# Optimization experiments

Hardware: AMD Instinct MI355X
Metric: run time of the kernel (lower is better)

Reference implementation:

```python
import jax, jax.numpy as jnp
import numpy as np

B, F_SIZE, DIM = 2048, 32, 64
LAYER_SIZES = (128, 128)


def setup_inputs() -> dict:
    key = jax.random.key(0)
    k1, k2, k3 = jax.random.split(key, 3)
    inputs = jax.random.normal(k1, (B, F_SIZE, DIM), dtype=jnp.float32)
    # Conv1d(kernel=1) weights: (out_channels, in_channels)
    W0 = jax.random.normal(k2, (128, F_SIZE * F_SIZE), dtype=jnp.float32) * 0.03
    b0 = jnp.zeros((128,), dtype=jnp.float32)
    # split_half -> field_nums[1] = 64 -> in_channels = 64 * 32 = 2048
    W1 = jax.random.normal(k3, (128, 64 * F_SIZE), dtype=jnp.float32) * 0.03
    b1 = jnp.zeros((128,), dtype=jnp.float32)
    return {"inputs": inputs, "W0": W0, "b0": b0, "W1": W1, "b1": b1}


def _cin_forward(inputs, Ws, bs):
    batch, _, dim = inputs.shape
    x0 = inputs
    h = inputs
    finals = []
    n_layers = len(Ws)
    for i in range(n_layers):
        H = h.shape[1]
        M = x0.shape[1]
        # outer-product interaction: (b, H, M, d) -> (b, H*M, d)
        z = jnp.einsum('bhd,bmd->bhmd', h, x0).reshape(batch, H * M, dim)
        # 1x1 conv == per-position channel matmul
        out = jnp.einsum('bcd,oc->bod', z, Ws[i]) + bs[i][None, :, None]
        out = jax.nn.relu(out)
        size = Ws[i].shape[0]
        if i != n_layers - 1:
            # split_half: first half feeds next layer, second half is output
            h = out[:, : size // 2, :]
            finals.append(out[:, size // 2 :, :])
        else:
            finals.append(out)
    result = jnp.concatenate(finals, axis=1)  # (b, 64 + 128, d)
    return jnp.sum(result, axis=-1)           # (b, 192)


def reference(inputs, W0, b0, W1, b1):
    return _cin_forward(inputs, (W0, W1), (b0, b1))
```

## Files before the change

kernel.cpp:

```cpp
#include <hip/hip_runtime.h>


#define BATCH 2048
#define FSZ   32
#define DIM   64
#define K0    1024
#define K1    2048
#define OUTC  192

#define W0_ELEMS (128 * K0)
#define W1_ELEMS (128 * K1)
#define TOT_ELEMS (W0_ELEMS + W1_ELEMS)
#define CVT_THREADS (TOT_ELEMS / 4)

typedef _Float16 v8h  __attribute__((ext_vector_type(8)));
typedef float    v16f __attribute__((ext_vector_type(16)));

#define XT_PITCH 40
#define XD_PITCH 66
#define HD_PITCH 66

__global__ void convert_w_kernel(const float* __restrict__ W0,
                                 const float* __restrict__ W1,
                                 _Float16* __restrict__ wsw) {
    int t = blockIdx.x * blockDim.x + threadIdx.x;
    if (t >= CVT_THREADS) return;
    int e = t * 4;
    const float* src;
    if (e < W0_ELEMS) {
        int f = e >> 3, j0 = e & 7;
        int ks = f >> 8, ob = (f >> 6) & 3, lane = f & 63;
        src = W0 + (size_t)(ob * 32 + (lane & 31)) * K0
                 + ks * 16 + (lane >> 5) * 8 + j0;
    } else {
        int u = e - W0_ELEMS;
        int f = u >> 3, j0 = u & 7;
        int ks = f >> 8, ob = (f >> 6) & 3, lane = f & 63;
        src = W1 + (size_t)(ob * 32 + (lane & 31)) * K1
                 + ks * 16 + (lane >> 5) * 8 + j0;
    }
    float4 v = *(const float4*)src;
    _Float16* dst = wsw + e;
    dst[0] = (_Float16)v.x;
    dst[1] = (_Float16)v.y;
    dst[2] = (_Float16)v.z;
    dst[3] = (_Float16)v.w;
}

__global__ __launch_bounds__(256, 4) void cin_kernel(
    const float* __restrict__ X,
    const float* __restrict__ b0,
    const float* __restrict__ b1,
    const _Float16* __restrict__ Wsw,
    float* __restrict__ out)
{
    __shared__ _Float16 xT[DIM * XT_PITCH];
    __shared__ _Float16 xD[FSZ * XD_PITCH];
    __shared__ _Float16 h1D[64 * HD_PITCH];

    const int b    = blockIdx.x;
    const int tid  = threadIdx.x;
    const int wave = tid >> 6;
    const int lane = tid & 63;
    const int half = lane >> 5;
    const int d0   = lane & 31;

    const float* xb = X + (size_t)b * (FSZ * DIM);
    #pragma unroll
    for (int i = tid; i < FSZ * DIM; i += 256) {
        int m = i >> 6, d = i & 63;
        _Float16 v = (_Float16)xb[i];
        xT[d * XT_PITCH + m] = v;
        xD[m * XD_PITCH + d] = v;
    }
    __syncthreads();

    v8h xh[2][2];
    #pragma unroll
    for (int db = 0; db < 2; ++db)
        #pragma unroll
        for (int p = 0; p < 2; ++p)
            xh[db][p] = *(const v8h*)(&xT[(db * 32 + d0) * XT_PITCH + p * 16 + half * 8]);

    v16f acc0 = (v16f)0.0f;
    v16f acc1 = (v16f)0.0f;

    {
        const _Float16* Wk = Wsw + (size_t)(wave * 64 + lane) * 8;
        #pragma unroll 4
        for (int ks = 0; ks < 64; ++ks) {
            v8h a = *(const v8h*)(Wk + (size_t)ks * 2048);
            const int hr = ks >> 1;
            _Float16 s0 = xD[hr * XD_PITCH + d0];
            _Float16 s1 = xD[hr * XD_PITCH + 32 + d0];
            v8h s08 = {s0, s0, s0, s0, s0, s0, s0, s0};
            v8h s18 = {s1, s1, s1, s1, s1, s1, s1, s1};
            v8h bf0 = s08 * xh[0][ks & 1];
            v8h bf1 = s18 * xh[1][ks & 1];
            acc0 = __builtin_amdgcn_mfma_f32_32x32x16_f16(a, bf0, acc0, 0, 0, 0);
            acc1 = __builtin_amdgcn_mfma_f32_32x32x16_f16(a, bf1, acc1, 0, 0, 0);
        }
    }

    if (wave < 2) {
        #pragma unroll
        for (int reg = 0; reg < 16; ++reg) {
            const int o = wave * 32 + (reg & 3) + 8 * (reg >> 2) + 4 * half;
            const float bias = b0[o];
            float v0 = acc0[reg] + bias; v0 = v0 > 0.0f ? v0 : 0.0f;
            float v1 = acc1[reg] + bias; v1 = v1 > 0.0f ? v1 : 0.0f;
            h1D[o * HD_PITCH + d0]      = (_Float16)v0;
            h1D[o * HD_PITCH + 32 + d0] = (_Float16)v1;
        }
    } else {
        #pragma unroll
        for (int reg = 0; reg < 16; ++reg) {
            const int o = wave * 32 + (reg & 3) + 8 * (reg >> 2) + 4 * half;
            const float bias = b0[o];
            float v0 = acc0[reg] + bias; v0 = v0 > 0.0f ? v0 : 0.0f;
            float v1 = acc1[reg] + bias; v1 = v1 > 0.0f ? v1 : 0.0f;
            float s = v0 + v1;
            s += __shfl_xor(s, 1);
            s += __shfl_xor(s, 2);
            s += __shfl_xor(s, 4);
            s += __shfl_xor(s, 8);
            s += __shfl_xor(s, 16);
            if (d0 == 0) out[(size_t)b * OUTC + (o - 64)] = s;
        }
    }
    __syncthreads();

    acc0 = (v16f)0.0f;
    acc1 = (v16f)0.0f;

    {
        const _Float16* Wk = Wsw + W0_ELEMS + (size_t)(wave * 64 + lane) * 8;
        #pragma unroll 4
        for (int ks = 0; ks < 128; ++ks) {
            v8h a = *(const v8h*)(Wk + (size_t)ks * 2048);
            const int hr = ks >> 1;
            _Float16 s0 = h1D[hr * HD_PITCH + d0];
            _Float16 s1 = h1D[hr * HD_PITCH + 32 + d0];
            v8h s08 = {s0, s0, s0, s0, s0, s0, s0, s0};
            v8h s18 = {s1, s1, s1, s1, s1, s1, s1, s1};
            v8h bf0 = s08 * xh[0][ks & 1];
            v8h bf1 = s18 * xh[1][ks & 1];
            acc0 = __builtin_amdgcn_mfma_f32_32x32x16_f16(a, bf0, acc0, 0, 0, 0);
            acc1 = __builtin_amdgcn_mfma_f32_32x32x16_f16(a, bf1, acc1, 0, 0, 0);
        }
    }

    #pragma unroll
    for (int reg = 0; reg < 16; ++reg) {
        const int o = wave * 32 + (reg & 3) + 8 * (reg >> 2) + 4 * half;
        const float bias = b1[o];
        float v0 = acc0[reg] + bias; v0 = v0 > 0.0f ? v0 : 0.0f;
        float v1 = acc1[reg] + bias; v1 = v1 > 0.0f ? v1 : 0.0f;
        float s = v0 + v1;
        s += __shfl_xor(s, 1);
        s += __shfl_xor(s, 2);
        s += __shfl_xor(s, 4);
        s += __shfl_xor(s, 8);
        s += __shfl_xor(s, 16);
        if (d0 == 0) out[(size_t)b * OUTC + 64 + o] = s;
    }
}

extern "C" void kernel_launch(void* const* d_in, const int* in_sizes, int n_in,
                              void* d_out, int out_size, void* d_ws, size_t ws_size,
                              hipStream_t stream) {
    const float* X  = (const float*)d_in[0];
    const float* W0 = (const float*)d_in[1];
    const float* b0 = (const float*)d_in[2];
    const float* W1 = (const float*)d_in[3];
    const float* b1 = (const float*)d_in[4];
    float* out = (float*)d_out;
    _Float16* wsw = (_Float16*)d_ws;

    convert_w_kernel<<<(CVT_THREADS + 255) / 256, 256, 0, stream>>>(W0, W1, wsw);
    cin_kernel<<<BATCH, 256, 0, stream>>>(X, b0, b1, wsw, out);
}
```

Measured before the change: 179.6 us.

## Process two batch items per block with 2x2 MFMA tiles and prefetched weights

Each block now handles two batch elements. Waves split by batch item and output-row half, and each wave computes a 2x2 grid of 32x32 MFMA tiles, so every weight fragment loaded from global memory is reused across two output slices. The weight layout is re-swizzled to match. Weight and scalar loads for the next k-step are software-prefetched into registers, and the LDS layouts for x and h1 are interleaved so each lane fetches both d-halves with a single packed load. The cost is twice as many accumulator registers and half as many blocks, which can lower occupancy and latency hiding.

```diff
diff --git a/kernel.cpp b/kernel.cpp
--- a/kernel.cpp
+++ b/kernel.cpp
@@ -13,12 +13,11 @@
 #define TOT_ELEMS (W0_ELEMS + W1_ELEMS)
 #define CVT_THREADS (TOT_ELEMS / 4)
 
-typedef _Float16 v8h  __attribute__((ext_vector_type(8)));
+typedef _Float16 v8h __attribute__((ext_vector_type(8)));
+typedef _Float16 v2h __attribute__((ext_vector_type(2)));
 typedef float    v16f __attribute__((ext_vector_type(16)));
 
 #define XT_PITCH 40
-#define XD_PITCH 66
-#define HD_PITCH 66
 
 __global__ void convert_w_kernel(const float* __restrict__ W0,
                                  const float* __restrict__ W1,
@@ -27,24 +26,28 @@
     if (t >= CVT_THREADS) return;
     int e = t * 4;
     const float* src;
+    _Float16* dst;
     if (e < W0_ELEMS) {
-        int f = e >> 3, j0 = e & 7;
-        int ks = f >> 8, ob = (f >> 6) & 3, lane = f & 63;
-        src = W0 + (size_t)(ob * 32 + (lane & 31)) * K0
+        int j0 = e & 7, lane = (e >> 3) & 63, s = (e >> 9) & 3, ks = e >> 11;
+        src = W0 + (size_t)(s * 32 + (lane & 31)) * K0
                  + ks * 16 + (lane >> 5) * 8 + j0;
+        dst = wsw + e;
     } else {
         int u = e - W0_ELEMS;
-        int f = u >> 3, j0 = u & 7;
-        int ks = f >> 8, ob = (f >> 6) & 3, lane = f & 63;
-        src = W1 + (size_t)(ob * 32 + (lane & 31)) * K1
+        int j0 = u & 7, lane = (u >> 3) & 63, s = (u >> 9) & 3, ks = u >> 11;
+        src = W1 + (size_t)(s * 32 + (lane & 31)) * K1
                  + ks * 16 + (lane >> 5) * 8 + j0;
+        dst = wsw + W0_ELEMS + u;
     }
     float4 v = *(const float4*)src;
-    _Float16* dst = wsw + e;
     dst[0] = (_Float16)v.x;
     dst[1] = (_Float16)v.y;
     dst[2] = (_Float16)v.z;
     dst[3] = (_Float16)v.w;
+}
+
+__device__ __forceinline__ v16f mfma32(v8h a, v8h b, v16f c) {
+    return __builtin_amdgcn_mfma_f32_32x32x16_f16(a, b, c, 0, 0, 0);
 }
 
 __global__ __launch_bounds__(256, 4) void cin_kernel(
@@ -54,115 +57,174 @@
     const _Float16* __restrict__ Wsw,
     float* __restrict__ out)
 {
-    __shared__ _Float16 xT[DIM * XT_PITCH];
-    __shared__ _Float16 xD[FSZ * XD_PITCH];
-    __shared__ _Float16 h1D[64 * HD_PITCH];
-
-    const int b    = blockIdx.x;
+    __shared__ _Float16 xT[2][DIM * XT_PITCH];
+    __shared__ _Float16 xP[2][FSZ * 64];
+    __shared__ _Float16 h1P[2][64 * 64];
+
+    const int b0i  = blockIdx.x * 2;
     const int tid  = threadIdx.x;
     const int wave = tid >> 6;
     const int lane = tid & 63;
-    const int half = lane >> 5;
+    const int p    = wave & 1;
+    const int rh   = wave >> 1;
     const int d0   = lane & 31;
-
-    const float* xb = X + (size_t)b * (FSZ * DIM);
+    const int hi   = lane >> 5;
+
     #pragma unroll
-    for (int i = tid; i < FSZ * DIM; i += 256) {
-        int m = i >> 6, d = i & 63;
-        _Float16 v = (_Float16)xb[i];
-        xT[d * XT_PITCH + m] = v;
-        xD[m * XD_PITCH + d] = v;
+    for (int i = 0; i < 4; ++i) {
+        int idx = tid + i * 256;
+        int pp = idx >> 9, r4 = idx & 511;
+        float4 v = *(const float4*)(X + (size_t)(b0i + pp) * (FSZ * DIM) + r4 * 4);
+        int m = (r4 * 4) >> 6, d = (r4 * 4) & 63;
+        int g = d >> 5, c = d & 31;
+        _Float16 f0 = (_Float16)v.x, f1 = (_Float16)v.y,
+                 f2 = (_Float16)v.z, f3 = (_Float16)v.w;
+        xT[pp][(d + 0) * XT_PITCH + m] = f0;
+        xT[pp][(d + 1) * XT_PITCH + m] = f1;
+        xT[pp][(d + 2) * XT_PITCH + m] = f2;
+        xT[pp][(d + 3) * XT_PITCH + m] = f3;
+        xP[pp][m * 64 + (c + 0) * 2 + g] = f0;
+        xP[pp][m * 64 + (c + 1) * 2 + g] = f1;
+        xP[pp][m * 64 + (c + 2) * 2 + g] = f2;
+        xP[pp][m * 64 + (c + 3) * 2 + g] = f3;
     }
     __syncthreads();
 
-    v8h xh[2][2];
+    v8h xw[2][2];
     #pragma unroll
-    for (int db = 0; db < 2; ++db)
-        #pragma unroll
-        for (int p = 0; p < 2; ++p)
-            xh[db][p] = *(const v8h*)(&xT[(db * 32 + d0) * XT_PITCH + p * 16 + half * 8]);
-
-    v16f acc0 = (v16f)0.0f;
-    v16f acc1 = (v16f)0.0f;
+    for (int g = 0; g < 2; ++g)
+        #pragma unroll
+        for (int q = 0; q < 2; ++q)
+            xw[g][q] = *(const v8h*)(&xT[p][(g * 32 + d0) * XT_PITCH + q * 16 + hi * 8]);
+
+    const _Float16* Wb0 = Wsw + (size_t)rh * 1024 + (size_t)lane * 8;
+    const _Float16* Wb1 = Wb0 + W0_ELEMS;
+    const _Float16* xPp = &xP[p][d0 * 2];
+    const _Float16* hPp = &h1P[p][d0 * 2];
+
+    v16f acc[2][2];
+    acc[0][0] = (v16f)0.0f; acc[0][1] = (v16f)0.0f;
+    acc[1][0] = (v16f)0.0f; acc[1][1] = (v16f)0.0f;
 
     {
-        const _Float16* Wk = Wsw + (size_t)(wave * 64 + lane) * 8;
-        #pragma unroll 4
-        for (int ks = 0; ks < 64; ++ks) {
-            v8h a = *(const v8h*)(Wk + (size_t)ks * 2048);
-            const int hr = ks >> 1;
-            _Float16 s0 = xD[hr * XD_PITCH + d0];
-            _Float16 s1 = xD[hr * XD_PITCH + 32 + d0];
+        v8h A0, A1, A2, A3, N0, N1, N2, N3;
+        v2h svC, svN;
+        A0 = *(const v8h*)(Wb0);        A1 = *(const v8h*)(Wb0 + 512);
+        A2 = *(const v8h*)(Wb0 + 2048); A3 = *(const v8h*)(Wb0 + 2560);
+        svC = *(const v2h*)(xPp);
+        #pragma unroll 1
+        for (int i = 0; i < 32; ++i) {
+            const int kn = (i + 1) & 31;
+            const _Float16* Wn = Wb0 + (size_t)kn * 4096;
+            N0 = *(const v8h*)(Wn);        N1 = *(const v8h*)(Wn + 512);
+            N2 = *(const v8h*)(Wn + 2048); N3 = *(const v8h*)(Wn + 2560);
+            svN = *(const v2h*)(xPp + kn * 64);
+            _Float16 s0 = svC[0], s1 = svC[1];
             v8h s08 = {s0, s0, s0, s0, s0, s0, s0, s0};
             v8h s18 = {s1, s1, s1, s1, s1, s1, s1, s1};
-            v8h bf0 = s08 * xh[0][ks & 1];
-            v8h bf1 = s18 * xh[1][ks & 1];
-            acc0 = __builtin_amdgcn_mfma_f32_32x32x16_f16(a, bf0, acc0, 0, 0, 0);
-            acc1 = __builtin_amdgcn_mfma_f32_32x32x16_f16(a, bf1, acc1, 0, 0, 0);
-        }
-    }
-
-    if (wave < 2) {
+            v8h be0 = s08 * xw[0][0];
+            v8h be1 = s18 * xw[1][0];
+            acc[0][0] = mfma32(A0, be0, acc[0][0]);
+            acc[1][0] = mfma32(A1, be0, acc[1][0]);
+            acc[0][1] = mfma32(A0, be1, acc[0][1]);
+            acc[1][1] = mfma32(A1, be1, acc[1][1]);
+            v8h bo0 = s08 * xw[0][1];
+            v8h bo1 = s18 * xw[1][1];
+            acc[0][0] = mfma32(A2, bo0, acc[0][0]);
+            acc[1][0] = mfma32(A3, bo0, acc[1][0]);
+            acc[0][1] = mfma32(A2, bo1, acc[0][1]);
+            acc[1][1] = mfma32(A3, bo1, acc[1][1]);
+            A0 = N0; A1 = N1; A2 = N2; A3 = N3;
+            svC = svN;
+        }
+    }
+
+    if (rh == 0) {
+        #pragma unroll
+        for (int sl = 0; sl < 2; ++sl) {
+            #pragma unroll
+            for (int reg = 0; reg < 16; ++reg) {
+                const int o = sl * 32 + (reg & 3) + 8 * (reg >> 2) + 4 * hi;
+                const float bias = b0[o];
+                float v0 = acc[sl][0][reg] + bias; v0 = v0 > 0.0f ? v0 : 0.0f;
+                float v1 = acc[sl][1][reg] + bias; v1 = v1 > 0.0f ? v1 : 0.0f;
+                v2h pk = {(_Float16)v0, (_Float16)v1};
+                *(v2h*)(&h1P[p][o * 64 + d0 * 2]) = pk;
+            }
+        }
+    } else {
+        #pragma unroll
+        for (int sl = 0; sl < 2; ++sl) {
+            #pragma unroll
+            for (int reg = 0; reg < 16; ++reg) {
+                const int o = 64 + sl * 32 + (reg & 3) + 8 * (reg >> 2) + 4 * hi;
+                const float bias = b0[o];
+                float v0 = acc[sl][0][reg] + bias; v0 = v0 > 0.0f ? v0 : 0.0f;
+                float v1 = acc[sl][1][reg] + bias; v1 = v1 > 0.0f ? v1 : 0.0f;
+                float s = v0 + v1;
+                s += __shfl_xor(s, 1);
+                s += __shfl_xor(s, 2);
+                s += __shfl_xor(s, 4);
+                s += __shfl_xor(s, 8);
+                s += __shfl_xor(s, 16);
+                if (d0 == 0) out[(size_t)(b0i + p) * OUTC + (o - 64)] = s;
+            }
+        }
+    }
+    __syncthreads();
+
+    acc[0][0] = (v16f)0.0f; acc[0][1] = (v16f)0.0f;
+    acc[1][0] = (v16f)0.0f; acc[1][1] = (v16f)0.0f;
+
+    {
+        v8h A0, A1, A2, A3, N0, N1, N2, N3;
+        v2h svC, svN;
+        A0 = *(const v8h*)(Wb1);        A1 = *(const v8h*)(Wb1 + 512);
+        A2 = *(const v8h*)(Wb1 + 2048); A3 = *(const v8h*)(Wb1 + 2560);
+        svC = *(const v2h*)(hPp);
+        #pragma unroll 1
+        for (int i = 0; i < 64; ++i) {
+            const int kn = (i + 1) & 63;
+            const _Float16* Wn = Wb1 + (size_t)kn * 4096;
+            N0 = *(const v8h*)(Wn);        N1 = *(const v8h*)(Wn + 512);
+            N2 = *(const v8h*)(Wn + 2048); N3 = *(const v8h*)(Wn + 2560);
+            svN = *(const v2h*)(hPp + kn * 64);
+            _Float16 s0 = svC[0], s1 = svC[1];
+            v8h s08 = {s0, s0, s0, s0, s0, s0, s0, s0};
+            v8h s18 = {s1, s1, s1, s1, s1, s1, s1, s1};
+            v8h be0 = s08 * xw[0][0];
+            v8h be1 = s18 * xw[1][0];
+            acc[0][0] = mfma32(A0, be0, acc[0][0]);
+            acc[1][0] = mfma32(A1, be0, acc[1][0]);
+            acc[0][1] = mfma32(A0, be1, acc[0][1]);
+            acc[1][1] = mfma32(A1, be1, acc[1][1]);
+            v8h bo0 = s08 * xw[0][1];
+            v8h bo1 = s18 * xw[1][1];
+            acc[0][0] = mfma32(A2, bo0, acc[0][0]);
+            acc[1][0] = mfma32(A3, bo0, acc[1][0]);
+            acc[0][1] = mfma32(A2, bo1, acc[0][1]);
+            acc[1][1] = mfma32(A3, bo1, acc[1][1]);
+            A0 = N0; A1 = N1; A2 = N2; A3 = N3;
+            svC = svN;
+        }
+    }
+
+    #pragma unroll
+    for (int sl = 0; sl < 2; ++sl) {
         #pragma unroll
         for (int reg = 0; reg < 16; ++reg) {
-            const int o = wave * 32 + (reg & 3) + 8 * (reg >> 2) + 4 * half;
-            const float bias = b0[o];
-            float v0 = acc0[reg] + bias; v0 = v0 > 0.0f ? v0 : 0.0f;
-            float v1 = acc1[reg] + bias; v1 = v1 > 0.0f ? v1 : 0.0f;
-            h1D[o * HD_PITCH + d0]      = (_Float16)v0;
-            h1D[o * HD_PITCH + 32 + d0] = (_Float16)v1;
-        }
-    } else {
-        #pragma unroll
-        for (int reg = 0; reg < 16; ++reg) {
-            const int o = wave * 32 + (reg & 3) + 8 * (reg >> 2) + 4 * half;
-            const float bias = b0[o];
-            float v0 = acc0[reg] + bias; v0 = v0 > 0.0f ? v0 : 0.0f;
-            float v1 = acc1[reg] + bias; v1 = v1 > 0.0f ? v1 : 0.0f;
+            const int o = rh * 64 + sl * 32 + (reg & 3) + 8 * (reg >> 2) + 4 * hi;
+            const float bias = b1[o];
+            float v0 = acc[sl][0][reg] + bias; v0 = v0 > 0.0f ? v0 : 0.0f;
+            float v1 = acc[sl][1][reg] + bias; v1 = v1 > 0.0f ? v1 : 0.0f;
             float s = v0 + v1;
             s += __shfl_xor(s, 1);
             s += __shfl_xor(s, 2);
             s += __shfl_xor(s, 4);
             s += __shfl_xor(s, 8);
             s += __shfl_xor(s, 16);
-            if (d0 == 0) out[(size_t)b * OUTC + (o - 64)] = s;
-        }
-    }
-    __syncthreads();
-
-    acc0 = (v16f)0.0f;
-    acc1 = (v16f)0.0f;
-
-    {
-        const _Float16* Wk = Wsw + W0_ELEMS + (size_t)(wave * 64 + lane) * 8;
-        #pragma unroll 4
-        for (int ks = 0; ks < 128; ++ks) {
-            v8h a = *(const v8h*)(Wk + (size_t)ks * 2048);
-            const int hr = ks >> 1;
-            _Float16 s0 = h1D[hr * HD_PITCH + d0];
-            _Float16 s1 = h1D[hr * HD_PITCH + 32 + d0];
-            v8h s08 = {s0, s0, s0, s0, s0, s0, s0, s0};
-            v8h s18 = {s1, s1, s1, s1, s1, s1, s1, s1};
-            v8h bf0 = s08 * xh[0][ks & 1];
-            v8h bf1 = s18 * xh[1][ks & 1];
-            acc0 = __builtin_amdgcn_mfma_f32_32x32x16_f16(a, bf0, acc0, 0, 0, 0);
-            acc1 = __builtin_amdgcn_mfma_f32_32x32x16_f16(a, bf1, acc1, 0, 0, 0);
-        }
-    }
-
-    #pragma unroll
-    for (int reg = 0; reg < 16; ++reg) {
-        const int o = wave * 32 + (reg & 3) + 8 * (reg >> 2) + 4 * half;
-        const float bias = b1[o];
-        float v0 = acc0[reg] + bias; v0 = v0 > 0.0f ? v0 : 0.0f;
-        float v1 = acc1[reg] + bias; v1 = v1 > 0.0f ? v1 : 0.0f;
-        float s = v0 + v1;
-        s += __shfl_xor(s, 1);
-        s += __shfl_xor(s, 2);
-        s += __shfl_xor(s, 4);
-        s += __shfl_xor(s, 8);
-        s += __shfl_xor(s, 16);
-        if (d0 == 0) out[(size_t)b * OUTC + 64 + o] = s;
+            if (d0 == 0) out[(size_t)(b0i + p) * OUTC + 64 + o] = s;
+        }
     }
 }
 
@@ -178,5 +240,5 @@
     _Float16* wsw = (_Float16*)d_ws;
 
     convert_w_kernel<<<(CVT_THREADS + 255) / 256, 256, 0, stream>>>(W0, W1, wsw);
-    cin_kernel<<<BATCH, 256, 0, stream>>>(X, b0, b1, wsw, out);
-}
+    cin_kernel<<<BATCH / 2, 256, 0, stream>>>(X, b0, b1, wsw, out);
+}
```

Measured after the change: 178.5 us. No clear change (-0.6%).
